# Optimization experiments

Hardware: AMD Instinct MI355X
Metric: run time of the kernel (lower is better)

The kernel has to match this reference:

```python
import jax, jax.numpy as jnp
import numpy as np

ALPHA_LEAKY = 0.2
EPS = 1e-10


def setup_inputs() -> dict:
    key = jax.random.key(0)
    k1, k2, k3, k4 = jax.random.split(key, 4)
    N, E, IN_DIM, OUT_DIM = 50000, 800000, 128, 64
    node_features = jax.random.normal(k1, (N, IN_DIM), dtype=jnp.float32)
    edge_index = jax.random.randint(k2, (2, E), 0, N, dtype=jnp.int64)
    # xavier_uniform with gain=1.414
    def xavier(k, shape, gain=1.414):
        fan_in, fan_out = shape[1], shape[0]
        bound = gain * np.sqrt(6.0 / (fan_in + fan_out))
        return jax.random.uniform(k, shape, jnp.float32, -bound, bound)
    W = xavier(k3, (OUT_DIM, IN_DIM))          # nn.Linear weight layout [out, in]
    a = xavier(k4, (1, 2 * OUT_DIM))           # attention vector [1, 2*out]
    return {"node_features": node_features, "edge_index": edge_index, "W": W, "a": a}


def reference(node_features, edge_index, W, a):
    # h = W(node_features): [N, out_dim]
    h = node_features @ W.T
    num_nodes, out_dim = h.shape
    src = edge_index[0]
    tgt = edge_index[1]
    # a @ cat([h_src, h_tgt]) decomposes into per-node partial scores (no [E, 2d] concat)
    s_src = h @ a[0, :out_dim]   # [N]
    s_tgt = h @ a[0, out_dim:]   # [N]
    e = jax.nn.leaky_relu(s_src[src] + s_tgt[tgt], negative_slope=ALPHA_LEAKY)  # [E]
    # segment softmax over incoming edges of each target node
    e_max = jax.ops.segment_max(e, tgt, num_segments=num_nodes)
    e_exp = jnp.exp(e - e_max[tgt])
    e_sum = jax.ops.segment_sum(e_exp, tgt, num_segments=num_nodes)
    attention = e_exp / (e_sum[tgt] + EPS)
    # weighted scatter-add aggregation of source features into targets
    h_prime = jax.ops.segment_sum(h[src] * attention[:, None], tgt, num_segments=num_nodes)
    return jax.nn.elu(h_prime)
```

## Files before the change

kernel.cpp:

```cpp
#include <hip/hip_runtime.h>
#include <math.h>

#define ALPHA_LEAKY 0.2f
#define EPS_F 1e-10f
#define NBMAX 1024
#define NBLK 256
#define CAP  4096

typedef __attribute__((ext_vector_type(8))) short short8;
typedef __attribute__((ext_vector_type(4))) float f32x4;

__device__ __forceinline__ unsigned short bf16_rne(float f) {
    unsigned u = __float_as_uint(f);
    u += 0x7FFFu + ((u >> 16) & 1u);
    return (unsigned short)(u >> 16);
}

__global__ void k_prep(const float* __restrict__ W, uint4* __restrict__ Wbf) {
    int f = blockIdx.x * 256 + threadIdx.x;
    int nt = f >> 8;
    if (nt >= 4) return;
    int l = f & 63, kt = (f >> 6) & 3;
    int nn = nt * 16 + (l & 15);
    int k  = kt * 32 + (l >> 4) * 8;
    const float* wr = W + nn * 128 + k;
    unsigned short b[8];
    #pragma unroll
    for (int j = 0; j < 8; ++j) b[j] = bf16_rne(wr[j]);
    uint4 v;
    v.x = (unsigned)b[0] | ((unsigned)b[1] << 16);
    v.y = (unsigned)b[2] | ((unsigned)b[3] << 16);
    v.z = (unsigned)b[4] | ((unsigned)b[5] << 16);
    v.w = (unsigned)b[6] | ((unsigned)b[7] << 16);
    Wbf[f] = v;
}

__global__ __launch_bounds__(256) void k_gemm(
    const float* __restrict__ X, const uint4* __restrict__ Wbf,
    const float* __restrict__ a, unsigned short* __restrict__ hb,
    float* __restrict__ s_src, float* __restrict__ s_tgt, int n, int nstripes) {
    const int lane = threadIdx.x & 63;
    const int ml = lane & 15, g = lane >> 4;
    short8 bfr[4][4];
    #pragma unroll
    for (int nt = 0; nt < 4; ++nt)
        #pragma unroll
        for (int kt = 0; kt < 4; ++kt) {
            uint4 v = Wbf[(nt * 4 + kt) * 64 + lane];
            bfr[nt][kt] = *(short8*)&v;
        }
    float as[4], at[4];
    #pragma unroll
    for (int nt = 0; nt < 4; ++nt) {
        as[nt] = a[nt * 16 + ml];
        at[nt] = a[64 + nt * 16 + ml];
    }
    for (int stripe = blockIdx.x * 4 + (threadIdx.x >> 6); stripe < nstripes;
         stripe += gridDim.x * 4) {
        const int row0 = stripe * 16;
        const int rrow = min(row0 + ml, n - 1);
        const float* xr = X + (size_t)rrow * 128;
        f32x4 acc[4] = {{0.f,0.f,0.f,0.f},{0.f,0.f,0.f,0.f},
                        {0.f,0.f,0.f,0.f},{0.f,0.f,0.f,0.f}};
        #pragma unroll
        for (int kt = 0; kt < 4; ++kt) {
            float4 x0 = *(const float4*)(xr + kt * 32 + g * 8);
            float4 x1 = *(const float4*)(xr + kt * 32 + g * 8 + 4);
            short8 af;
            af[0] = (short)bf16_rne(x0.x); af[1] = (short)bf16_rne(x0.y);
            af[2] = (short)bf16_rne(x0.z); af[3] = (short)bf16_rne(x0.w);
            af[4] = (short)bf16_rne(x1.x); af[5] = (short)bf16_rne(x1.y);
            af[6] = (short)bf16_rne(x1.z); af[7] = (short)bf16_rne(x1.w);
            #pragma unroll
            for (int nt = 0; nt < 4; ++nt)
                acc[nt] = __builtin_amdgcn_mfma_f32_16x16x32_bf16(
                    af, bfr[nt][kt], acc[nt], 0, 0, 0);
        }
        #pragma unroll
        for (int reg = 0; reg < 4; ++reg) {
            int row = row0 + g * 4 + reg;
            float p = acc[0][reg] * as[0] + acc[1][reg] * as[1] +
                      acc[2][reg] * as[2] + acc[3][reg] * as[3];
            float q = acc[0][reg] * at[0] + acc[1][reg] * at[1] +
                      acc[2][reg] * at[2] + acc[3][reg] * at[3];
            #pragma unroll
            for (int off = 1; off < 16; off <<= 1) {
                p += __shfl_xor(p, off, 64);
                q += __shfl_xor(q, off, 64);
            }
            if (ml == 0 && row < n) { s_src[row] = p; s_tgt[row] = q; }
        }
        #pragma unroll
        for (int nt = 0; nt < 4; ++nt)
            #pragma unroll
            for (int reg = 0; reg < 4; ++reg) {
                int row = row0 + g * 4 + reg;
                if (row < n)
                    hb[(size_t)row * 64 + nt * 16 + ml] = bf16_rne(acc[nt][reg]);
            }
    }
}

__global__ __launch_bounds__(256) void k_hist(
    const int* __restrict__ ei, int* __restrict__ histg, int nb, int E, int epb) {
    __shared__ int hist[NBMAX];
    const int t = threadIdx.x;
    for (int k = t; k < nb; k += 256) hist[k] = 0;
    __syncthreads();
    const int e0 = blockIdx.x * epb, e1 = min(e0 + epb, E);
    for (int e = e0 + t; e < e1; e += 256)
        atomicAdd(&hist[ei[E + e] >> 6], 1);
    __syncthreads();
    int* outp = histg + (size_t)blockIdx.x * nb;
    for (int k = t; k < nb; k += 256) outp[k] = hist[k];
}

__global__ __launch_bounds__(256) void k_colscan(
    int* __restrict__ histg, int* __restrict__ btot, int nb) {
    __shared__ int wsum[4];
    const int bucket = blockIdx.x;
    const int t = threadIdx.x, lane = t & 63, w = t >> 6;
    int v = histg[(size_t)t * nb + bucket];
    int pre = v;
    #pragma unroll
    for (int off = 1; off < 64; off <<= 1) {
        int x = __shfl_up(pre, off, 64);
        if (lane >= off) pre += x;
    }
    if (lane == 63) wsum[w] = pre;
    __syncthreads();
    int wb = 0;
    for (int k = 0; k < w; ++k) wb += wsum[k];
    histg[(size_t)t * nb + bucket] = wb + pre - v;
    if (t == 255) btot[bucket] = wb + pre;
}

__global__ __launch_bounds__(256) void k_bscan(
    const int* __restrict__ btot, int* __restrict__ bstart, int nb, int E) {
    __shared__ int wsum[4];
    int t = threadIdx.x;
    int lane = t & 63, w = t >> 6;
    int v[4]; int sum = 0;
    #pragma unroll
    for (int j = 0; j < 4; ++j) {
        int idx = t * 4 + j;
        v[j] = (idx < nb) ? btot[idx] : 0;
        sum += v[j];
    }
    int pre = sum;
    #pragma unroll
    for (int off = 1; off < 64; off <<= 1) {
        int x = __shfl_up(pre, off, 64);
        if (lane >= off) pre += x;
    }
    if (lane == 63) wsum[w] = pre;
    __syncthreads();
    int wbase = 0;
    for (int k = 0; k < w; ++k) wbase += wsum[k];
    int run = wbase + pre - sum;
    #pragma unroll
    for (int j = 0; j < 4; ++j) {
        int idx = t * 4 + j;
        if (idx < nb) bstart[idx] = run;
        run += v[j];
    }
    if (t == 255) bstart[nb] = E;
}

__global__ __launch_bounds__(256) void k_place(
    const int* __restrict__ ei, const int* __restrict__ histg,
    const int* __restrict__ bstart, unsigned* __restrict__ st,
    int nb, int E, int epb) {
    __shared__ int cur[NBMAX];
    const int t = threadIdx.x;
    const int* my = histg + (size_t)blockIdx.x * nb;
    for (int k = t; k < nb; k += 256) cur[k] = bstart[k] + my[k];
    __syncthreads();
    const int e0 = blockIdx.x * epb, e1 = min(e0 + epb, E);
    for (int e = e0 + t; e < e1; e += 256) {
        int s  = ei[e];
        int tt = ei[E + e];
        int slot = atomicAdd(&cur[tt >> 6], 1);
        st[slot] = ((unsigned)s << 6) | (unsigned)(tt & 63);
    }
}

__device__ __forceinline__ void accum8(float acc[8], uint4 hv, float w) {
    unsigned u[4] = {hv.x, hv.y, hv.z, hv.w};
    #pragma unroll
    for (int i = 0; i < 4; ++i) {
        float lo = __uint_as_float(u[i] << 16);
        float hi = __uint_as_float(u[i] & 0xFFFF0000u);
        acc[2 * i]     = fmaf(w, lo, acc[2 * i]);
        acc[2 * i + 1] = fmaf(w, hi, acc[2 * i + 1]);
    }
}

__global__ __launch_bounds__(256) void k_bnode2(
    const unsigned* __restrict__ st, const int* __restrict__ bstart,
    const float* __restrict__ s_src, const float* __restrict__ s_tgt,
    const unsigned short* __restrict__ hb, float* __restrict__ out, int n) {
    __shared__ int st_lds[CAP];
    __shared__ int hist[64];
    __shared__ int base_lds[64];
    __shared__ int deg_lds[64];
    __shared__ int cur[64];
    __shared__ float stgt_lds[64];
    const int b = blockIdx.x;
    const int n0 = b << 6;
    const int t = threadIdx.x;
    const int lane = t & 63;
    const int w = t >> 6;
    const int g = lane >> 3, r = lane & 7;
    const int s0 = bstart[b], seg = bstart[b + 1] - s0;

    if (t < 64) {
        hist[t] = 0;
        int node = n0 + t;
        stgt_lds[t] = (node < n) ? s_tgt[node] : 0.f;
    }
    __syncthreads();

    if (seg <= CAP) {
        unsigned mine[16];
        #pragma unroll
        for (int j = 0; j < 16; ++j) {
            int i = t + j * 256;
            mine[j] = 0xFFFFFFFFu;
            if (i < seg) {
                unsigned p = st[s0 + i];
                mine[j] = p;
                atomicAdd(&hist[p & 63u], 1);
            }
        }
        __syncthreads();
        if (t < 64) {
            int v = hist[t];
            int pre = v;
            #pragma unroll
            for (int off = 1; off < 64; off <<= 1) {
                int x = __shfl_up(pre, off, 64);
                if (t >= off) pre += x;
            }
            int bs = pre - v;
            base_lds[t] = bs;
            deg_lds[t] = v;
            cur[t] = bs;
        }
        __syncthreads();
        #pragma unroll
        for (int j = 0; j < 16; ++j) {
            if (mine[j] != 0xFFFFFFFFu) {
                int slot = atomicAdd(&cur[mine[j] & 63u], 1);
                st_lds[slot] = (int)(mine[j] >> 6);
            }
        }
        __syncthreads();

        for (int nl = w * 16; nl < w * 16 + 16; ++nl) {
            const int node = n0 + nl;
            const int bb = base_lds[nl];
            const int d = deg_lds[nl];
            const float stg = stgt_lds[nl];
            float acc[8] = {0.f,0.f,0.f,0.f,0.f,0.f,0.f,0.f};
            if (d <= 64) {
                int src_l = 0; float v = -INFINITY;
                if (lane < d) {
                    src_l = st_lds[bb + lane];
                    float x = s_src[src_l] + stg;
                    v = (x > 0.f) ? x : ALPHA_LEAKY * x;
                }
                float m = v;
                #pragma unroll
                for (int off = 32; off > 0; off >>= 1) m = fmaxf(m, __shfl_xor(m, off, 64));
                float ex = (lane < d) ? expf(v - m) : 0.f;
                float sum = ex;
                #pragma unroll
                for (int off = 32; off > 0; off >>= 1) sum += __shfl_xor(sum, off, 64);
                float w_l = ex * (1.f / (sum + EPS_F));
                for (int k = 0; k < d; k += 8) {
                    int ke = k + g;
                    int s    = __shfl(src_l, ke, 64);
                    float wv = __shfl(w_l,  ke, 64);
                    uint4 hv = ((const uint4*)(hb + (size_t)s * 64))[r];
                    accum8(acc, hv, wv);
                }
            } else {
                float m = -INFINITY;
                for (int c = lane; c < d; c += 64) {
                    float x = s_src[st_lds[bb + c]] + stg;
                    x = (x > 0.f) ? x : ALPHA_LEAKY * x;
                    m = fmaxf(m, x);
                }
                #pragma unroll
                for (int off = 32; off > 0; off >>= 1) m = fmaxf(m, __shfl_xor(m, off, 64));
                float sum = 0.f;
                for (int c = lane; c < d; c += 64) {
                    float x = s_src[st_lds[bb + c]] + stg;
                    x = (x > 0.f) ? x : ALPHA_LEAKY * x;
                    sum += expf(x - m);
                }
                #pragma unroll
                for (int off = 32; off > 0; off >>= 1) sum += __shfl_xor(sum, off, 64);
                float inv = 1.f / (sum + EPS_F);
                for (int c0 = 0; c0 < d; c0 += 64) {
                    int j = c0 + lane;
                    int src_l = 0; float w_l = 0.f;
                    if (j < d) {
                        src_l = st_lds[bb + j];
                        float x = s_src[src_l] + stg;
                        x = (x > 0.f) ? x : ALPHA_LEAKY * x;
                        w_l = expf(x - m) * inv;
                    }
                    int lim = min(64, d - c0);
                    for (int k = 0; k < lim; k += 8) {
                        int ke = k + g;
                        int s    = __shfl(src_l, ke, 64);
                        float wv = __shfl(w_l,  ke, 64);
                        uint4 hv = ((const uint4*)(hb + (size_t)s * 64))[r];
                        accum8(acc, hv, wv);
                    }
                }
            }
            #pragma unroll
            for (int off = 8; off <= 32; off <<= 1) {
                #pragma unroll
                for (int j = 0; j < 8; ++j) acc[j] += __shfl_xor(acc[j], off, 64);
            }
            if (g == 0 && node < n) {
                float4 o0, o1;
                o0.x = acc[0] > 0.f ? acc[0] : expf(acc[0]) - 1.f;
                o0.y = acc[1] > 0.f ? acc[1] : expf(acc[1]) - 1.f;
                o0.z = acc[2] > 0.f ? acc[2] : expf(acc[2]) - 1.f;
                o0.w = acc[3] > 0.f ? acc[3] : expf(acc[3]) - 1.f;
                o1.x = acc[4] > 0.f ? acc[4] : expf(acc[4]) - 1.f;
                o1.y = acc[5] > 0.f ? acc[5] : expf(acc[5]) - 1.f;
                o1.z = acc[6] > 0.f ? acc[6] : expf(acc[6]) - 1.f;
                o1.w = acc[7] > 0.f ? acc[7] : expf(acc[7]) - 1.f;
                float4* o4 = (float4*)out + (size_t)node * 16;
                o4[r * 2]     = o0;
                o4[r * 2 + 1] = o1;
            }
        }
    } else {
        for (int nl = w * 16; nl < w * 16 + 16; ++nl) {
            const int node = n0 + nl;
            if (node >= n) continue;
            const float stg = stgt_lds[nl];
            float m = -INFINITY;
            for (int c = lane; c < seg; c += 64) {
                unsigned p = st[s0 + c];
                if ((int)(p & 63u) == nl) {
                    float x = s_src[p >> 6] + stg;
                    x = (x > 0.f) ? x : ALPHA_LEAKY * x;
                    m = fmaxf(m, x);
                }
            }
            #pragma unroll
            for (int off = 32; off > 0; off >>= 1) m = fmaxf(m, __shfl_xor(m, off, 64));
            float sum = 0.f;
            for (int c = lane; c < seg; c += 64) {
                unsigned p = st[s0 + c];
                if ((int)(p & 63u) == nl) {
                    float x = s_src[p >> 6] + stg;
                    x = (x > 0.f) ? x : ALPHA_LEAKY * x;
                    sum += expf(x - m);
                }
            }
            #pragma unroll
            for (int off = 32; off > 0; off >>= 1) sum += __shfl_xor(sum, off, 64);
            float inv = 1.f / (sum + EPS_F);
            float acc[8] = {0.f,0.f,0.f,0.f,0.f,0.f,0.f,0.f};
            for (int c0 = 0; c0 < seg; c0 += 64) {
                int j = c0 + lane;
                int src_l = 0; float w_l = 0.f;
                if (j < seg) {
                    unsigned p = st[s0 + j];
                    if ((int)(p & 63u) == nl) {
                        src_l = p >> 6;
                        float x = s_src[src_l] + stg;
                        x = (x > 0.f) ? x : ALPHA_LEAKY * x;
                        w_l = expf(x - m) * inv;
                    }
                }
                int lim = min(64, seg - c0);
                for (int k = 0; k < lim; k += 8) {
                    int ke = k + g;
                    int s    = __shfl(src_l, ke, 64);
                    float wv = __shfl(w_l,  ke, 64);
                    uint4 hv = ((const uint4*)(hb + (size_t)s * 64))[r];
                    accum8(acc, hv, wv);
                }
            }
            #pragma unroll
            for (int off = 8; off <= 32; off <<= 1) {
                #pragma unroll
                for (int j = 0; j < 8; ++j) acc[j] += __shfl_xor(acc[j], off, 64);
            }
            if (g == 0) {
                float4 o0, o1;
                o0.x = acc[0] > 0.f ? acc[0] : expf(acc[0]) - 1.f;
                o0.y = acc[1] > 0.f ? acc[1] : expf(acc[1]) - 1.f;
                o0.z = acc[2] > 0.f ? acc[2] : expf(acc[2]) - 1.f;
                o0.w = acc[3] > 0.f ? acc[3] : expf(acc[3]) - 1.f;
                o1.x = acc[4] > 0.f ? acc[4] : expf(acc[4]) - 1.f;
                o1.y = acc[5] > 0.f ? acc[5] : expf(acc[5]) - 1.f;
                o1.z = acc[6] > 0.f ? acc[6] : expf(acc[6]) - 1.f;
                o1.w = acc[7] > 0.f ? acc[7] : expf(acc[7]) - 1.f;
                float4* o4 = (float4*)out + (size_t)node * 16;
                o4[r * 2]     = o0;
                o4[r * 2 + 1] = o1;
            }
        }
    }
}

extern "C" void kernel_launch(void* const* d_in, const int* in_sizes, int n_in,
                              void* d_out, int out_size, void* d_ws, size_t ws_size,
                              hipStream_t stream) {
    const float* X  = (const float*)d_in[0];
    const int*   ei = (const int*)d_in[1];
    const float* W  = (const float*)d_in[2];
    const float* a  = (const float*)d_in[3];
    float* out = (float*)d_out;

    const int N = in_sizes[0] / 128;
    const int E = in_sizes[1] / 2;
    const int nb = (N + 63) >> 6;
    const int epb = (E + NBLK - 1) / NBLK;

    char* p = (char*)d_ws;
    unsigned short* hb = (unsigned short*)p; p += (size_t)N * 64 * sizeof(unsigned short);
    uint4*    Wbf    = (uint4*)p;    p += 1024 * sizeof(uint4);
    float*    s_src  = (float*)p;    p += (size_t)N * sizeof(float);
    float*    s_tgt  = (float*)p;    p += (size_t)N * sizeof(float);
    int*      histg  = (int*)p;      p += (size_t)NBLK * nb * sizeof(int);
    int*      btot   = (int*)p;      p += (size_t)nb * sizeof(int);
    int*      bstart = (int*)p;      p += (size_t)(nb + 1) * sizeof(int);
    unsigned* st     = (unsigned*)p;

    const int nstripes = (N + 15) / 16;
    k_prep   <<<4, 256, 0, stream>>>(W, Wbf);
    k_gemm   <<<(nstripes + 3) / 4, 256, 0, stream>>>(X, Wbf, a, hb, s_src, s_tgt, N, nstripes);
    k_hist   <<<NBLK, 256, 0, stream>>>(ei, histg, nb, E, epb);
    k_colscan<<<nb, 256, 0, stream>>>(histg, btot, nb);
    k_bscan  <<<1, 256, 0, stream>>>(btot, bstart, nb, E);
    k_place  <<<NBLK, 256, 0, stream>>>(ei, histg, bstart, st, nb, E, epb);
    k_bnode2 <<<nb, 256, 0, stream>>>(st, bstart, s_src, s_tgt, hb, out, N);
}
```

Before: 158.3 us.

## Halve node buckets to 32 and fuse bucket scans with last-block counter

Buckets now cover 32 target nodes instead of 64. This doubles the number of aggregation blocks and gives each wave 8 nodes, spreading the gather work more evenly across CUs. The column scan and global bucket scan are merged into one kernel, where the last finishing block, detected through an atomic counter, performs the final prefix scan, removing a launch. In exchange, the histogram arrays grow and the per-block LDS edge capacity is halved, so more buckets may take the slow path.

```diff
diff --git a/kernel.cpp b/kernel.cpp
--- a/kernel.cpp
+++ b/kernel.cpp
@@ -3,9 +3,9 @@
 
 #define ALPHA_LEAKY 0.2f
 #define EPS_F 1e-10f
-#define NBMAX 1024
+#define NBMAX 2048
 #define NBLK 256
-#define CAP  4096
+#define CAP  2048
 
 typedef __attribute__((ext_vector_type(8))) short short8;
 typedef __attribute__((ext_vector_type(4))) float f32x4;
@@ -102,22 +102,26 @@
 }
 
 __global__ __launch_bounds__(256) void k_hist(
-    const int* __restrict__ ei, int* __restrict__ histg, int nb, int E, int epb) {
+    const int* __restrict__ ei, int* __restrict__ histg, int* __restrict__ done,
+    int nb, int E, int epb) {
     __shared__ int hist[NBMAX];
     const int t = threadIdx.x;
+    if (blockIdx.x == 0 && t == 0) atomicExch(done, 0);
     for (int k = t; k < nb; k += 256) hist[k] = 0;
     __syncthreads();
     const int e0 = blockIdx.x * epb, e1 = min(e0 + epb, E);
     for (int e = e0 + t; e < e1; e += 256)
-        atomicAdd(&hist[ei[E + e] >> 6], 1);
+        atomicAdd(&hist[ei[E + e] >> 5], 1);
     __syncthreads();
     int* outp = histg + (size_t)blockIdx.x * nb;
     for (int k = t; k < nb; k += 256) outp[k] = hist[k];
 }
 
-__global__ __launch_bounds__(256) void k_colscan(
-    int* __restrict__ histg, int* __restrict__ btot, int nb) {
+__global__ __launch_bounds__(256) void k_scan(
+    int* __restrict__ histg, int* __restrict__ btot, int* __restrict__ bstart,
+    int* __restrict__ done, int nb, int E) {
     __shared__ int wsum[4];
+    __shared__ int lastflag;
     const int bucket = blockIdx.x;
     const int t = threadIdx.x, lane = t & 63, w = t >> 6;
     int v = histg[(size_t)t * nb + bucket];
@@ -132,37 +136,38 @@
     int wb = 0;
     for (int k = 0; k < w; ++k) wb += wsum[k];
     histg[(size_t)t * nb + bucket] = wb + pre - v;
-    if (t == 255) btot[bucket] = wb + pre;
-}
-
-__global__ __launch_bounds__(256) void k_bscan(
-    const int* __restrict__ btot, int* __restrict__ bstart, int nb, int E) {
-    __shared__ int wsum[4];
-    int t = threadIdx.x;
-    int lane = t & 63, w = t >> 6;
-    int v[4]; int sum = 0;
-    #pragma unroll
-    for (int j = 0; j < 4; ++j) {
-        int idx = t * 4 + j;
-        v[j] = (idx < nb) ? btot[idx] : 0;
-        sum += v[j];
-    }
-    int pre = sum;
+    if (t == 255) atomicExch(&btot[bucket], wb + pre);
+    __syncthreads();
+    if (t == 0) {
+        __threadfence();
+        lastflag = (atomicAdd(done, 1) == nb - 1) ? 1 : 0;
+    }
+    __syncthreads();
+    if (!lastflag) return;
+    __threadfence();
+    int tv[8]; int sum = 0;
+    #pragma unroll
+    for (int j = 0; j < 8; ++j) {
+        int idx = t * 8 + j;
+        tv[j] = (idx < nb) ? atomicAdd(&btot[idx], 0) : 0;
+        sum += tv[j];
+    }
+    int p2 = sum;
     #pragma unroll
     for (int off = 1; off < 64; off <<= 1) {
-        int x = __shfl_up(pre, off, 64);
-        if (lane >= off) pre += x;
-    }
-    if (lane == 63) wsum[w] = pre;
-    __syncthreads();
-    int wbase = 0;
-    for (int k = 0; k < w; ++k) wbase += wsum[k];
-    int run = wbase + pre - sum;
-    #pragma unroll
-    for (int j = 0; j < 4; ++j) {
-        int idx = t * 4 + j;
+        int x = __shfl_up(p2, off, 64);
+        if (lane >= off) p2 += x;
+    }
+    if (lane == 63) wsum[w] = p2;
+    __syncthreads();
+    int wb2 = 0;
+    for (int k = 0; k < w; ++k) wb2 += wsum[k];
+    int run = wb2 + p2 - sum;
+    #pragma unroll
+    for (int j = 0; j < 8; ++j) {
+        int idx = t * 8 + j;
         if (idx < nb) bstart[idx] = run;
-        run += v[j];
+        run += tv[j];
     }
     if (t == 255) bstart[nb] = E;
 }
@@ -180,8 +185,8 @@
     for (int e = e0 + t; e < e1; e += 256) {
         int s  = ei[e];
         int tt = ei[E + e];
-        int slot = atomicAdd(&cur[tt >> 6], 1);
-        st[slot] = ((unsigned)s << 6) | (unsigned)(tt & 63);
+        int slot = atomicAdd(&cur[tt >> 5], 1);
+        st[slot] = ((unsigned)s << 5) | (unsigned)(tt & 31);
     }
 }
 
@@ -201,20 +206,20 @@
     const float* __restrict__ s_src, const float* __restrict__ s_tgt,
     const unsigned short* __restrict__ hb, float* __restrict__ out, int n) {
     __shared__ int st_lds[CAP];
-    __shared__ int hist[64];
-    __shared__ int base_lds[64];
-    __shared__ int deg_lds[64];
-    __shared__ int cur[64];
-    __shared__ float stgt_lds[64];
+    __shared__ int hist[32];
+    __shared__ int base_lds[32];
+    __shared__ int deg_lds[32];
+    __shared__ int cur[32];
+    __shared__ float stgt_lds[32];
     const int b = blockIdx.x;
-    const int n0 = b << 6;
+    const int n0 = b << 5;
     const int t = threadIdx.x;
     const int lane = t & 63;
     const int w = t >> 6;
     const int g = lane >> 3, r = lane & 7;
     const int s0 = bstart[b], seg = bstart[b + 1] - s0;
 
-    if (t < 64) {
+    if (t < 32) {
         hist[t] = 0;
         int node = n0 + t;
         stgt_lds[t] = (node < n) ? s_tgt[node] : 0.f;
@@ -222,23 +227,23 @@
     __syncthreads();
 
     if (seg <= CAP) {
-        unsigned mine[16];
-        #pragma unroll
-        for (int j = 0; j < 16; ++j) {
+        unsigned mine[8];
+        #pragma unroll
+        for (int j = 0; j < 8; ++j) {
             int i = t + j * 256;
             mine[j] = 0xFFFFFFFFu;
             if (i < seg) {
                 unsigned p = st[s0 + i];
                 mine[j] = p;
-                atomicAdd(&hist[p & 63u], 1);
+                atomicAdd(&hist[p & 31u], 1);
             }
         }
         __syncthreads();
-        if (t < 64) {
+        if (t < 32) {
             int v = hist[t];
             int pre = v;
             #pragma unroll
-            for (int off = 1; off < 64; off <<= 1) {
+            for (int off = 1; off < 32; off <<= 1) {
                 int x = __shfl_up(pre, off, 64);
                 if (t >= off) pre += x;
             }
@@ -249,15 +254,15 @@
         }
         __syncthreads();
         #pragma unroll
-        for (int j = 0; j < 16; ++j) {
+        for (int j = 0; j < 8; ++j) {
             if (mine[j] != 0xFFFFFFFFu) {
-                int slot = atomicAdd(&cur[mine[j] & 63u], 1);
-                st_lds[slot] = (int)(mine[j] >> 6);
+                int slot = atomicAdd(&cur[mine[j] & 31u], 1);
+                st_lds[slot] = (int)(mine[j] >> 5);
             }
         }
         __syncthreads();
 
-        for (int nl = w * 16; nl < w * 16 + 16; ++nl) {
+        for (int nl = w * 8; nl < w * 8 + 8; ++nl) {
             const int node = n0 + nl;
             const int bb = base_lds[nl];
             const int d = deg_lds[nl];
@@ -343,15 +348,15 @@
             }
         }
     } else {
-        for (int nl = w * 16; nl < w * 16 + 16; ++nl) {
+        for (int nl = w * 8; nl < w * 8 + 8; ++nl) {
             const int node = n0 + nl;
             if (node >= n) continue;
             const float stg = stgt_lds[nl];
             float m = -INFINITY;
             for (int c = lane; c < seg; c += 64) {
                 unsigned p = st[s0 + c];
-                if ((int)(p & 63u) == nl) {
-                    float x = s_src[p >> 6] + stg;
+                if ((int)(p & 31u) == nl) {
+                    float x = s_src[p >> 5] + stg;
                     x = (x > 0.f) ? x : ALPHA_LEAKY * x;
                     m = fmaxf(m, x);
                 }
@@ -361,8 +366,8 @@
             float sum = 0.f;
             for (int c = lane; c < seg; c += 64) {
                 unsigned p = st[s0 + c];
-                if ((int)(p & 63u) == nl) {
-                    float x = s_src[p >> 6] + stg;
+                if ((int)(p & 31u) == nl) {
+                    float x = s_src[p >> 5] + stg;
                     x = (x > 0.f) ? x : ALPHA_LEAKY * x;
                     sum += expf(x - m);
                 }
@@ -376,8 +381,8 @@
                 int src_l = 0; float w_l = 0.f;
                 if (j < seg) {
                     unsigned p = st[s0 + j];
-                    if ((int)(p & 63u) == nl) {
-                        src_l = p >> 6;
+                    if ((int)(p & 31u) == nl) {
+                        src_l = p >> 5;
                         float x = s_src[src_l] + stg;
                         x = (x > 0.f) ? x : ALPHA_LEAKY * x;
                         w_l = expf(x - m) * inv;
@@ -426,7 +431,7 @@
 
     const int N = in_sizes[0] / 128;
     const int E = in_sizes[1] / 2;
-    const int nb = (N + 63) >> 6;
+    const int nb = (N + 31) >> 5;
     const int epb = (E + NBLK - 1) / NBLK;
 
     char* p = (char*)d_ws;
@@ -437,14 +442,14 @@
     int*      histg  = (int*)p;      p += (size_t)NBLK * nb * sizeof(int);
     int*      btot   = (int*)p;      p += (size_t)nb * sizeof(int);
     int*      bstart = (int*)p;      p += (size_t)(nb + 1) * sizeof(int);
+    int*      done   = (int*)p;      p += 4 * sizeof(int);
     unsigned* st     = (unsigned*)p;
 
     const int nstripes = (N + 15) / 16;
-    k_prep   <<<4, 256, 0, stream>>>(W, Wbf);
-    k_gemm   <<<(nstripes + 3) / 4, 256, 0, stream>>>(X, Wbf, a, hb, s_src, s_tgt, N, nstripes);
-    k_hist   <<<NBLK, 256, 0, stream>>>(ei, histg, nb, E, epb);
-    k_colscan<<<nb, 256, 0, stream>>>(histg, btot, nb);
-    k_bscan  <<<1, 256, 0, stream>>>(btot, bstart, nb, E);
-    k_place  <<<NBLK, 256, 0, stream>>>(ei, histg, bstart, st, nb, E, epb);
-    k_bnode2 <<<nb, 256, 0, stream>>>(st, bstart, s_src, s_tgt, hb, out, N);
-}
+    k_prep  <<<4, 256, 0, stream>>>(W, Wbf);
+    k_gemm  <<<(nstripes + 3) / 4, 256, 0, stream>>>(X, Wbf, a, hb, s_src, s_tgt, N, nstripes);
+    k_hist  <<<NBLK, 256, 0, stream>>>(ei, histg, done, nb, E, epb);
+    k_scan  <<<nb, 256, 0, stream>>>(histg, btot, bstart, done, nb, E);
+    k_place <<<NBLK, 256, 0, stream>>>(ei, histg, bstart, st, nb, E, epb);
+    k_bnode2<<<nb, 256, 0, stream>>>(st, bstart, s_src, s_tgt, hb, out, N);
+}
```

New measurement: 219.3 us. 38.6% more time.
